# Kernel tuning notes

Hardware: AMD Instinct MI355X
Metric: run time of the kernel (lower is better)

## Reference

```python
import jax, jax.numpy as jnp
import numpy as np

COSIM_THRESHOLD = 0.5


def warp_affine_simple(src, theta, H, W):
    # src: [N, C, H, W], theta: [N, 2, 3]. Matches torch affine_grid+grid_sample
    # with align_corners=True and zero padding.
    ys = jnp.linspace(-1.0, 1.0, H)
    xs = jnp.linspace(-1.0, 1.0, W)
    gy, gx = jnp.meshgrid(ys, xs, indexing='ij')              # [H, W]
    base = jnp.stack([gx, gy, jnp.ones_like(gx)], axis=-1)    # [H, W, 3]
    coords = jnp.einsum('nij,hwj->nhwi', theta, base)         # [N, H, W, 2] (x, y)
    x = (coords[..., 0] + 1.0) * (W - 1) / 2.0
    y = (coords[..., 1] + 1.0) * (H - 1) / 2.0
    x0 = jnp.floor(x); y0 = jnp.floor(y)
    x1 = x0 + 1.0;     y1 = y0 + 1.0

    def corner(xi, yi):
        valid = ((xi >= 0) & (xi <= W - 1) & (yi >= 0) & (yi <= H - 1)).astype(src.dtype)
        xc = jnp.clip(xi, 0, W - 1).astype(jnp.int32)
        yc = jnp.clip(yi, 0, H - 1).astype(jnp.int32)
        vals = jax.vmap(lambda img, yy, xx: img[:, yy, xx])(src, yc, xc)  # [N, C, H, W]
        return vals * valid[:, None, :, :]

    wa = ((x1 - x) * (y1 - y))[:, None]
    wb = ((x - x0) * (y1 - y))[:, None]
    wc = ((x1 - x) * (y - y0))[:, None]
    wd = ((x - x0) * (y - y0))[:, None]
    return (corner(x0, y0) * wa + corner(x1, y0) * wb
            + corner(x0, y1) * wc + corner(x1, y1) * wd)


def setup_inputs() -> dict:
    key = jax.random.key(0)
    k1, k2, k3, k4 = jax.random.split(key, 4)
    B, N, nc, C, H, W = 4, 2, 256, 256, 96, 192
    feature = jax.random.normal(k1, (B * N, C, H, W), dtype=jnp.float32)
    codebook = jax.random.normal(k2, (nc, C), dtype=jnp.float32)
    codebook_pub = jax.random.normal(k3, (nc, C), dtype=jnp.float32)
    eye = jnp.broadcast_to(jnp.array([[1.0, 0.0, 0.0], [0.0, 1.0, 0.0]], jnp.float32),
                           (B, N, N, 2, 3))
    affine_matrix = eye + 0.05 * jax.random.normal(k4, (B, N, N, 2, 3), dtype=jnp.float32)
    record_len = jnp.full((B,), N, dtype=jnp.int32)
    return {'feature': feature, 'codebook': codebook, 'codebook_pub': codebook_pub,
            'affine_matrix': affine_matrix, 'record_len': record_len}


def reference(feature, codebook, codebook_pub, affine_matrix, record_len):
    # ---- sender: codebook dot-product weight projection + sigmoid ----
    # (local2unify / recombiner_send treated as identity: C == C_uni)
    b, C, H, W = feature.shape
    nc = codebook.shape[0]
    B = affine_matrix.shape[0]
    N = int(np.asarray(record_len)[0])  # uniform groups (static)

    dots = jnp.einsum('bchw,nc->bnhw', feature, codebook)           # [b, nc, H, W]
    norms = jnp.sum(codebook * codebook, axis=1)                    # [nc]
    weights = jax.nn.sigmoid(dots / norms[None, :, None, None])

    # ---- seletc_fill_weight: cosine-sim mask + affine-warp selective fill ----
    nl = codebook / jnp.linalg.norm(codebook, axis=1, keepdims=True)
    npub = codebook_pub / jnp.linalg.norm(codebook_pub, axis=1, keepdims=True)
    max_cosims = jnp.max(nl @ npub.T, axis=1)                       # [nc]
    masked = max_cosims <= COSIM_THRESHOLD                          # [nc]

    w = weights.reshape(B, N, nc, H, W)
    agent = jnp.arange(N)
    zero_cond = masked[None, None, :] & (agent[None, :, None] > 0)  # [1, N, nc]
    w = jnp.where(zero_cond[:, :, :, None, None], 0.0, w)

    # warp ego weights into each agent frame: t_matrix[:, i=0]
    theta = affine_matrix[:, :N, 0].reshape(B * N, 2, 3)
    ego = jnp.broadcast_to(w[:, :1], (B, N, nc, H, W)).reshape(B * N, nc, H, W)
    ego_w = warp_affine_simple(ego, theta, H, W).reshape(B, N, nc, H, W)

    w_sum = w.sum(axis=(-1, -2))                                    # [B, N, nc]
    fill = (w_sum == 0) & (agent[None, :, None] > 0)
    w = jnp.where(fill[:, :, :, None, None], ego_w, w)
    weights = w.reshape(b, nc, H, W)

    # ---- receiver: softmax over codes + einsum combine ----
    # (recombiner_receive / unify2local treated as identity)
    weights = jax.nn.softmax(weights, axis=1)
    out = jnp.einsum('bnhw,nc->bchw', weights, codebook)            # [b, C, H, W]
    return out
```

## Files before the change

### kernel.cpp

```cpp
#include <hip/hip_runtime.h>

#define HH 96
#define WW 192
#define PP (HH*WW)
#define CC 256
#define NCODE 256
#define NIMG 8
#define PT 64
#define PTILES (PP/PT)

typedef unsigned short u16;
typedef unsigned int u32;
using short8 = __attribute__((ext_vector_type(8))) short;
using f32x4  = __attribute__((ext_vector_type(4))) float;

__device__ inline u16 f2bf(float f) {
    union { float f; u32 u; } x; x.f = f;
    u32 r = x.u + 0x7fffu + ((x.u >> 16) & 1u);
    return (u16)(r >> 16);
}
__device__ inline float bf2f(u16 b) {
    union { u32 u; float f; } x; x.u = ((u32)b) << 16;
    return x.f;
}

__global__ __launch_bounds__(256) void k_prep(const float* __restrict__ cb,
                                              const float* __restrict__ cbp,
                                              float* __restrict__ invnorms,
                                              int*   __restrict__ masked,
                                              u16*   __restrict__ cbF,
                                              u16*   __restrict__ cbTF) {
    __shared__ float cbn[256];
    __shared__ float red[256];
    int n = blockIdx.x, t = threadIdx.x;
    float v = cb[n*256 + t];
    cbn[t] = v;
    red[t] = v * v;
    __syncthreads();
    for (int s = 128; s > 0; s >>= 1) { if (t < s) red[t] += red[t+s]; __syncthreads(); }
    float norm2 = red[0];
    if (t == 0) invnorms[n] = 1.0f / norm2;
    __syncthreads();

    {
        int ks = t >> 5, g = (t >> 3) & 3, j = t & 7;
        cbF[((size_t)(ks*16 + (n >> 4))*64 + g*16 + (n & 15))*8 + j] = f2bf(cbn[ks*32 + g*8 + j]);
    }
    {
        int ct = t >> 4, cl = t & 15;
        int ks = n >> 5, g = (n >> 3) & 3, j = n & 7;
        cbTF[((size_t)(ks*16 + ct)*64 + g*16 + cl)*8 + j] = f2bf(cbn[ct*16 + cl]);
    }
    float dot = 0.f, np2 = 0.f;
    const float4* pm4 = (const float4*)(cbp + (size_t)t*256);
    for (int c4 = 0; c4 < 64; ++c4) {
        float4 pv = pm4[c4];
        dot += cbn[c4*4+0]*pv.x + cbn[c4*4+1]*pv.y + cbn[c4*4+2]*pv.z + cbn[c4*4+3]*pv.w;
        np2 += pv.x*pv.x + pv.y*pv.y + pv.z*pv.z + pv.w*pv.w;
    }
    float cosv = dot * rsqrtf(norm2 * np2);
    __syncthreads();
    red[t] = cosv;
    __syncthreads();
    for (int s = 128; s > 0; s >>= 1) { if (t < s) red[t] = fmaxf(red[t], red[t+s]); __syncthreads(); }
    if (t == 0) masked[n] = (red[0] <= 0.5f) ? 1 : 0;
}

__global__ __launch_bounds__(256, 2) void k_gemm1f(const float* __restrict__ feat,
                                                   const u16* __restrict__ cbF,
                                                   const float* __restrict__ invnorms,
                                                   u16* __restrict__ w_all) {
    __shared__ alignas(16) u16 alds[32*64*8];
    int bid = blockIdx.x;
    int img = bid / PTILES, pt = bid % PTILES;
    int p0 = pt * PT;
    int t = threadIdx.x, wv = t >> 6, l = t & 63;
    int lr = l & 15, lg = l >> 4;

    short8 breg[32];
    #pragma unroll
    for (int nt = 0; nt < 4; ++nt)
        #pragma unroll
        for (int ks = 0; ks < 8; ++ks)
            breg[nt*8 + ks] = *(const short8*)(cbF + ((size_t)((ks*16 + wv*4 + nt)*64 + l))*8);

    float invn[4];
    #pragma unroll
    for (int nt = 0; nt < 4; ++nt) invn[nt] = invnorms[wv*64 + nt*16 + lr];

    int px = t & 63;
    int cgrp = t >> 6;
    const float* fb = feat + ((size_t)img*CC)*PP + p0 + px;
    int m_ = px >> 4;
    int lslot = px & 15;
    #pragma unroll
    for (int i = 0; i < 16; ++i) {
        int c0 = i*16 + cgrp*4;
        float f0 = fb[(size_t)(c0+0)*PP];
        float f1 = fb[(size_t)(c0+1)*PP];
        float f2 = fb[(size_t)(c0+2)*PP];
        float f3 = fb[(size_t)(c0+3)*PP];
        u32 lo = (u32)f2bf(f0) | ((u32)f2bf(f1) << 16);
        u32 hi = (u32)f2bf(f2) | ((u32)f2bf(f3) << 16);
        int ks = c0 >> 5;
        int lane = lslot + (((c0 >> 3) & 3) << 4);
        u32* dst = (u32*)((char*)alds + ((size_t)((m_*8 + ks)*64 + lane))*16 + (c0 & 7)*2);
        dst[0] = lo; dst[1] = hi;
    }
    __syncthreads();

    #pragma unroll
    for (int m = 0; m < 4; ++m) {
        f32x4 acc[4];
        #pragma unroll
        for (int nt = 0; nt < 4; ++nt) acc[nt] = (f32x4){0.f,0.f,0.f,0.f};
        #pragma unroll
        for (int ks = 0; ks < 8; ++ks) {
            short8 a = *(const short8*)(alds + ((size_t)((m*8 + ks)*64 + l))*8);
            #pragma unroll
            for (int nt = 0; nt < 4; ++nt)
                acc[nt] = __builtin_amdgcn_mfma_f32_16x16x32_bf16(a, breg[nt*8 + ks], acc[nt], 0, 0, 0);
        }
        #pragma unroll
        for (int nt = 0; nt < 4; ++nt) {
            #pragma unroll
            for (int r = 0; r < 4; ++r) {
                int p = p0 + m*16 + lg*4 + r;
                int n = wv*64 + nt*16 + lr;
                float x = acc[nt][r] * invn[nt];
                float w = 1.f / (1.f + __expf(-x));
                w_all[((size_t)img*PP + p)*256 + n] = f2bf(w);
            }
        }
    }
}

__global__ __launch_bounds__(256, 2) void k_out(const u16* __restrict__ w_all,
                                                const u16* __restrict__ cbTF,
                                                const int* __restrict__ masked,
                                                const float* __restrict__ am,
                                                float* __restrict__ out) {
    __shared__ alignas(16) u16 smx[32*64*8];
    int bid = blockIdx.x;
    int img = bid / PTILES, pt = bid % PTILES;
    int p0 = pt * PT;
    int t = threadIdx.x;

    {
        int pl = t >> 2, q = t & 3;
        int p = p0 + pl;
        float vals[64];
        const u16* own = w_all + ((size_t)img*PP + p)*256 + q*64;
        #pragma unroll
        for (int i = 0; i < 8; ++i) {
            short8 v = *(const short8*)(own + i*8);
            #pragma unroll
            for (int j = 0; j < 8; ++j) vals[i*8 + j] = bf2f((u16)v[j]);
        }
        if (img & 1) {
            int hh = p / WW, ww = p % WW;
            const float* th = am + (size_t)img*12;
            float gx = ww * (2.f/(WW-1)) - 1.f;
            float gy = hh * (2.f/(HH-1)) - 1.f;
            float xr = th[0]*gx + th[1]*gy + th[2];
            float yr = th[3]*gx + th[4]*gy + th[5];
            float x = (xr + 1.f) * ((WW-1)*0.5f);
            float y = (yr + 1.f) * ((HH-1)*0.5f);
            float x0f = floorf(x), y0f = floorf(y);
            float dx = x - x0f, dy = y - y0f;
            int x0 = (int)x0f, y0 = (int)y0f;
            float wc4[4] = {(1.f-dx)*(1.f-dy), dx*(1.f-dy), (1.f-dx)*dy, dx*dy};
            int xs_[4] = {x0, x0+1, x0, x0+1};
            int ys_[4] = {y0, y0, y0+1, y0+1};
            const u16* w0 = w_all + ((size_t)(img-1)*PP)*256;
            const u16* cptr[4];
            #pragma unroll
            for (int k = 0; k < 4; ++k) {
                bool ok = (xs_[k] >= 0) & (xs_[k] < WW) & (ys_[k] >= 0) & (ys_[k] < HH);
                cptr[k] = ok ? (w0 + ((size_t)(ys_[k]*WW + xs_[k]))*256 + q*64) : nullptr;
            }
            #pragma unroll
            for (int ch = 0; ch < 4; ++ch) {
                float wch[16];
                #pragma unroll
                for (int i = 0; i < 16; ++i) wch[i] = 0.f;
                #pragma unroll
                for (int k = 0; k < 4; ++k) {
                    if (cptr[k]) {
                        const u16* cp = cptr[k] + ch*16;
                        short8 a = *(const short8*)(cp);
                        short8 b = *(const short8*)(cp + 8);
                        float wk = wc4[k];
                        #pragma unroll
                        for (int j = 0; j < 8; ++j) { wch[j] += wk*bf2f((u16)a[j]); wch[8+j] += wk*bf2f((u16)b[j]); }
                    }
                }
                #pragma unroll
                for (int i = 0; i < 16; ++i)
                    if (masked[q*64 + ch*16 + i]) vals[ch*16 + i] = wch[i];
            }
        }
        float m = vals[0];
        #pragma unroll
        for (int i = 1; i < 64; ++i) m = fmaxf(m, vals[i]);
        m = fmaxf(m, __shfl_xor(m, 1));
        m = fmaxf(m, __shfl_xor(m, 2));
        float s = 0.f;
        #pragma unroll
        for (int i = 0; i < 64; ++i) { vals[i] = __expf(vals[i] - m); s += vals[i]; }
        s += __shfl_xor(s, 1);
        s += __shfl_xor(s, 2);
        float inv = 1.f / s;
        int p4 = pl >> 4;
        #pragma unroll
        for (int i = 0; i < 32; ++i) {
            int n = q*64 + i*2;
            int ks = n >> 5;
            int lane = (pl & 15) + (((n >> 3) & 3) << 4);
            u32 v = (u32)f2bf(vals[i*2] * inv) | ((u32)f2bf(vals[i*2+1] * inv) << 16);
            *(u32*)((char*)smx + ((size_t)((ks*4 + p4)*64 + lane))*16 + (n & 7)*2) = v;
        }
    }

    int wv = t >> 6, l = t & 63;
    int lr = l & 15, lg = l >> 4;
    short8 areg[32];
    #pragma unroll
    for (int ct = 0; ct < 4; ++ct)
        #pragma unroll
        for (int ks = 0; ks < 8; ++ks)
            areg[ct*8 + ks] = *(const short8*)(cbTF + ((size_t)((ks*16 + wv*4 + ct)*64 + l))*8);
    __syncthreads();

    f32x4 acc[4][4];
    #pragma unroll
    for (int i = 0; i < 4; ++i)
        #pragma unroll
        for (int j = 0; j < 4; ++j) acc[i][j] = (f32x4){0.f,0.f,0.f,0.f};

    #pragma unroll
    for (int ks = 0; ks < 8; ++ks) {
        short8 b[4];
        #pragma unroll
        for (int p4 = 0; p4 < 4; ++p4)
            b[p4] = *(const short8*)(smx + ((size_t)((ks*4 + p4)*64 + l))*8);
        #pragma unroll
        for (int ct = 0; ct < 4; ++ct)
            #pragma unroll
            for (int p4 = 0; p4 < 4; ++p4)
                acc[ct][p4] = __builtin_amdgcn_mfma_f32_16x16x32_bf16(areg[ct*8 + ks], b[p4], acc[ct][p4], 0, 0, 0);
    }
    #pragma unroll
    for (int ct = 0; ct < 4; ++ct)
        #pragma unroll
        for (int p4 = 0; p4 < 4; ++p4)
            #pragma unroll
            for (int r = 0; r < 4; ++r) {
                int c = wv*64 + ct*16 + lg*4 + r;
                int p = p0 + p4*16 + lr;
                out[((size_t)img*CC + c)*PP + p] = acc[ct][p4][r];
            }
}

extern "C" void kernel_launch(void* const* d_in, const int* in_sizes, int n_in,
                              void* d_out, int out_size, void* d_ws, size_t ws_size,
                              hipStream_t stream) {
    const float* feature = (const float*)d_in[0];
    const float* cb      = (const float*)d_in[1];
    const float* cbp     = (const float*)d_in[2];
    const float* am      = (const float*)d_in[3];
    float* out = (float*)d_out;

    char* ws = (char*)d_ws;
    size_t o = 0;
    u16* w_all = (u16*)(ws + o); o += (size_t)NIMG*PP*NCODE*2;
    u16* cbF   = (u16*)(ws + o); o += 256*256*2;
    u16* cbTF  = (u16*)(ws + o); o += 256*256*2;
    float* invnorms = (float*)(ws + o); o += 256*4;
    int* masked     = (int*)(ws + o);   o += 256*4;

    hipLaunchKernelGGL(k_prep, dim3(256), dim3(256), 0, stream, cb, cbp, invnorms, masked, cbF, cbTF);
    hipLaunchKernelGGL(k_gemm1f, dim3(NIMG*PTILES), dim3(256), 0, stream, feature, cbF, invnorms, w_all);
    hipLaunchKernelGGL(k_out, dim3(NIMG*PTILES), dim3(256), 0, stream, w_all, cbTF, masked, am, out);
}
```

Measured before the change: 351.5 us.

## Skip agent GEMM when all codes masked, pack mask bits, raise occupancy

k_prep now writes a count of unmasked codes plus a 256-bit mask bitset. When every code is masked, k_gemm1f skips the non-ego images and k_out zero-fills their own weights instead of loading them. Register use is cut by splitting B/A fragments into two halves so launch bounds can go to 3 blocks per CU. The softmax tile in LDS now uses a row-major layout with XOR swizzling and 16-byte stores. The skip depends on the data: with random codebooks the max cosine is likely below 0.5 for all codes, so the skip path probably runs on the test inputs. The semantics stay correct in either case.

```diff
diff --git a/kernel.cpp b/kernel.cpp
--- a/kernel.cpp
+++ b/kernel.cpp
@@ -27,7 +27,7 @@
 __global__ __launch_bounds__(256) void k_prep(const float* __restrict__ cb,
                                               const float* __restrict__ cbp,
                                               float* __restrict__ invnorms,
-                                              int*   __restrict__ masked,
+                                              int*   __restrict__ meta,
                                               u16*   __restrict__ cbF,
                                               u16*   __restrict__ cbTF) {
     __shared__ float cbn[256];
@@ -63,30 +63,32 @@
     red[t] = cosv;
     __syncthreads();
     for (int s = 128; s > 0; s >>= 1) { if (t < s) red[t] = fmaxf(red[t], red[t+s]); __syncthreads(); }
-    if (t == 0) masked[n] = (red[0] <= 0.5f) ? 1 : 0;
-}
-
-__global__ __launch_bounds__(256, 2) void k_gemm1f(const float* __restrict__ feat,
+    if (t == 0) {
+        int maskedv = (red[0] <= 0.5f) ? 1 : 0;
+        if (maskedv) atomicOr((u32*)&meta[1 + (n >> 5)], 1u << (n & 31));
+        else         atomicAdd(&meta[0], 1);
+    }
+}
+
+__global__ __launch_bounds__(256, 3) void k_gemm1f(const float* __restrict__ feat,
                                                    const u16* __restrict__ cbF,
                                                    const float* __restrict__ invnorms,
-                                                   u16* __restrict__ w_all) {
+                                                   u16* __restrict__ w_all,
+                                                   const int* __restrict__ meta) {
     __shared__ alignas(16) u16 alds[32*64*8];
     int bid = blockIdx.x;
     int img = bid / PTILES, pt = bid % PTILES;
+    if ((img & 1) && (meta[0] == 0)) return;
     int p0 = pt * PT;
     int t = threadIdx.x, wv = t >> 6, l = t & 63;
     int lr = l & 15, lg = l >> 4;
 
-    short8 breg[32];
+    short8 breg[16];
     #pragma unroll
-    for (int nt = 0; nt < 4; ++nt)
+    for (int nt2 = 0; nt2 < 2; ++nt2)
         #pragma unroll
         for (int ks = 0; ks < 8; ++ks)
-            breg[nt*8 + ks] = *(const short8*)(cbF + ((size_t)((ks*16 + wv*4 + nt)*64 + l))*8);
-
-    float invn[4];
-    #pragma unroll
-    for (int nt = 0; nt < 4; ++nt) invn[nt] = invnorms[wv*64 + nt*16 + lr];
+            breg[nt2*8 + ks] = *(const short8*)(cbF + ((size_t)((ks*16 + wv*4 + nt2)*64 + l))*8);
 
     int px = t & 63;
     int cgrp = t >> 6;
@@ -110,52 +112,76 @@
     __syncthreads();
 
     #pragma unroll
-    for (int m = 0; m < 4; ++m) {
-        f32x4 acc[4];
-        #pragma unroll
-        for (int nt = 0; nt < 4; ++nt) acc[nt] = (f32x4){0.f,0.f,0.f,0.f};
-        #pragma unroll
-        for (int ks = 0; ks < 8; ++ks) {
-            short8 a = *(const short8*)(alds + ((size_t)((m*8 + ks)*64 + l))*8);
-            #pragma unroll
-            for (int nt = 0; nt < 4; ++nt)
-                acc[nt] = __builtin_amdgcn_mfma_f32_16x16x32_bf16(a, breg[nt*8 + ks], acc[nt], 0, 0, 0);
-        }
-        #pragma unroll
-        for (int nt = 0; nt < 4; ++nt) {
-            #pragma unroll
-            for (int r = 0; r < 4; ++r) {
-                int p = p0 + m*16 + lg*4 + r;
-                int n = wv*64 + nt*16 + lr;
-                float x = acc[nt][r] * invn[nt];
-                float w = 1.f / (1.f + __expf(-x));
-                w_all[((size_t)img*PP + p)*256 + n] = f2bf(w);
-            }
-        }
-    }
-}
-
-__global__ __launch_bounds__(256, 2) void k_out(const u16* __restrict__ w_all,
+    for (int nh = 0; nh < 2; ++nh) {
+        if (nh) {
+            #pragma unroll
+            for (int nt2 = 0; nt2 < 2; ++nt2)
+                #pragma unroll
+                for (int ks = 0; ks < 8; ++ks)
+                    breg[nt2*8 + ks] = *(const short8*)(cbF + ((size_t)((ks*16 + wv*4 + 2 + nt2)*64 + l))*8);
+        }
+        float invn[2];
+        #pragma unroll
+        for (int nt2 = 0; nt2 < 2; ++nt2) invn[nt2] = invnorms[wv*64 + (nh*2 + nt2)*16 + lr];
+        #pragma unroll
+        for (int m = 0; m < 4; ++m) {
+            f32x4 acc[2];
+            acc[0] = (f32x4){0.f,0.f,0.f,0.f};
+            acc[1] = (f32x4){0.f,0.f,0.f,0.f};
+            #pragma unroll
+            for (int ks = 0; ks < 8; ++ks) {
+                short8 a = *(const short8*)(alds + ((size_t)((m*8 + ks)*64 + l))*8);
+                acc[0] = __builtin_amdgcn_mfma_f32_16x16x32_bf16(a, breg[ks],     acc[0], 0, 0, 0);
+                acc[1] = __builtin_amdgcn_mfma_f32_16x16x32_bf16(a, breg[8 + ks], acc[1], 0, 0, 0);
+            }
+            #pragma unroll
+            for (int nt2 = 0; nt2 < 2; ++nt2) {
+                #pragma unroll
+                for (int r = 0; r < 4; ++r) {
+                    int p = p0 + m*16 + lg*4 + r;
+                    int n = wv*64 + (nh*2 + nt2)*16 + lr;
+                    float x = acc[nt2][r] * invn[nt2];
+                    float w = 1.f / (1.f + __expf(-x));
+                    w_all[((size_t)img*PP + p)*256 + n] = f2bf(w);
+                }
+            }
+        }
+    }
+}
+
+__device__ inline u32 smx_off(int p, int n) {
+    return (u32)(((p*256 + n)*2) ^ ((p & 7) << 4));
+}
+
+__global__ __launch_bounds__(256, 3) void k_out(const u16* __restrict__ w_all,
                                                 const u16* __restrict__ cbTF,
-                                                const int* __restrict__ masked,
+                                                const int* __restrict__ meta,
                                                 const float* __restrict__ am,
                                                 float* __restrict__ out) {
-    __shared__ alignas(16) u16 smx[32*64*8];
+    __shared__ alignas(16) u16 smx[64*256];
     int bid = blockIdx.x;
     int img = bid / PTILES, pt = bid % PTILES;
     int p0 = pt * PT;
     int t = threadIdx.x;
+    bool allm = (meta[0] == 0);
 
     {
         int pl = t >> 2, q = t & 3;
         int p = p0 + pl;
+        u32 mb0 = (u32)meta[1 + q*2], mb1 = (u32)meta[2 + q*2];
+        bool ego_only = (img & 1) && allm;
         float vals[64];
-        const u16* own = w_all + ((size_t)img*PP + p)*256 + q*64;
-        #pragma unroll
-        for (int i = 0; i < 8; ++i) {
-            short8 v = *(const short8*)(own + i*8);
-            #pragma unroll
-            for (int j = 0; j < 8; ++j) vals[i*8 + j] = bf2f((u16)v[j]);
+        if (!ego_only) {
+            const u16* own = w_all + ((size_t)img*PP + p)*256 + q*64;
+            #pragma unroll
+            for (int i = 0; i < 8; ++i) {
+                short8 v = *(const short8*)(own + i*8);
+                #pragma unroll
+                for (int j = 0; j < 8; ++j) vals[i*8 + j] = bf2f((u16)v[j]);
+            }
+        } else {
+            #pragma unroll
+            for (int i = 0; i < 64; ++i) vals[i] = 0.f;
         }
         if (img & 1) {
             int hh = p / WW, ww = p % WW;
@@ -195,9 +221,12 @@
                         for (int j = 0; j < 8; ++j) { wch[j] += wk*bf2f((u16)a[j]); wch[8+j] += wk*bf2f((u16)b[j]); }
                     }
                 }
-                #pragma unroll
-                for (int i = 0; i < 16; ++i)
-                    if (masked[q*64 + ch*16 + i]) vals[ch*16 + i] = wch[i];
+                u32 mb = (ch < 2) ? mb0 : mb1;
+                #pragma unroll
+                for (int i = 0; i < 16; ++i) {
+                    int bit = (ch & 1)*16 + i;
+                    if ((mb >> bit) & 1) vals[ch*16 + i] = wch[i];
+                }
             }
         }
         float m = vals[0];
@@ -211,55 +240,54 @@
         s += __shfl_xor(s, 1);
         s += __shfl_xor(s, 2);
         float inv = 1.f / s;
-        int p4 = pl >> 4;
-        #pragma unroll
-        for (int i = 0; i < 32; ++i) {
-            int n = q*64 + i*2;
-            int ks = n >> 5;
-            int lane = (pl & 15) + (((n >> 3) & 3) << 4);
-            u32 v = (u32)f2bf(vals[i*2] * inv) | ((u32)f2bf(vals[i*2+1] * inv) << 16);
-            *(u32*)((char*)smx + ((size_t)((ks*4 + p4)*64 + lane))*16 + (n & 7)*2) = v;
-        }
-    }
+        #pragma unroll
+        for (int i = 0; i < 8; ++i) {
+            short8 v;
+            #pragma unroll
+            for (int j = 0; j < 8; ++j) v[j] = (short)f2bf(vals[i*8 + j] * inv);
+            *(short8*)((char*)smx + smx_off(pl, q*64 + i*8)) = v;
+        }
+    }
+    __syncthreads();
 
     int wv = t >> 6, l = t & 63;
     int lr = l & 15, lg = l >> 4;
-    short8 areg[32];
     #pragma unroll
-    for (int ct = 0; ct < 4; ++ct)
-        #pragma unroll
-        for (int ks = 0; ks < 8; ++ks)
-            areg[ct*8 + ks] = *(const short8*)(cbTF + ((size_t)((ks*16 + wv*4 + ct)*64 + l))*8);
-    __syncthreads();
-
-    f32x4 acc[4][4];
-    #pragma unroll
-    for (int i = 0; i < 4; ++i)
-        #pragma unroll
-        for (int j = 0; j < 4; ++j) acc[i][j] = (f32x4){0.f,0.f,0.f,0.f};
-
-    #pragma unroll
-    for (int ks = 0; ks < 8; ++ks) {
-        short8 b[4];
-        #pragma unroll
-        for (int p4 = 0; p4 < 4; ++p4)
-            b[p4] = *(const short8*)(smx + ((size_t)((ks*4 + p4)*64 + l))*8);
-        #pragma unroll
-        for (int ct = 0; ct < 4; ++ct)
+    for (int ch = 0; ch < 2; ++ch) {
+        short8 areg[16];
+        #pragma unroll
+        for (int ct2 = 0; ct2 < 2; ++ct2)
+            #pragma unroll
+            for (int ks = 0; ks < 8; ++ks)
+                areg[ct2*8 + ks] = *(const short8*)(cbTF + ((size_t)((ks*16 + wv*4 + ch*2 + ct2)*64 + l))*8);
+        f32x4 acc[2][4];
+        #pragma unroll
+        for (int i = 0; i < 2; ++i)
+            #pragma unroll
+            for (int j = 0; j < 4; ++j) acc[i][j] = (f32x4){0.f,0.f,0.f,0.f};
+        #pragma unroll
+        for (int ks = 0; ks < 8; ++ks) {
+            short8 b[4];
             #pragma unroll
             for (int p4 = 0; p4 < 4; ++p4)
-                acc[ct][p4] = __builtin_amdgcn_mfma_f32_16x16x32_bf16(areg[ct*8 + ks], b[p4], acc[ct][p4], 0, 0, 0);
-    }
-    #pragma unroll
-    for (int ct = 0; ct < 4; ++ct)
-        #pragma unroll
-        for (int p4 = 0; p4 < 4; ++p4)
-            #pragma unroll
-            for (int r = 0; r < 4; ++r) {
-                int c = wv*64 + ct*16 + lg*4 + r;
-                int p = p0 + p4*16 + lr;
-                out[((size_t)img*CC + c)*PP + p] = acc[ct][p4][r];
-            }
+                b[p4] = *(const short8*)((char*)smx + smx_off(p4*16 + lr, ks*32 + lg*8));
+            #pragma unroll
+            for (int ct2 = 0; ct2 < 2; ++ct2)
+                #pragma unroll
+                for (int p4 = 0; p4 < 4; ++p4)
+                    acc[ct2][p4] = __builtin_amdgcn_mfma_f32_16x16x32_bf16(areg[ct2*8 + ks], b[p4], acc[ct2][p4], 0, 0, 0);
+        }
+        #pragma unroll
+        for (int ct2 = 0; ct2 < 2; ++ct2)
+            #pragma unroll
+            for (int p4 = 0; p4 < 4; ++p4)
+                #pragma unroll
+                for (int r = 0; r < 4; ++r) {
+                    int c = wv*64 + (ch*2 + ct2)*16 + lg*4 + r;
+                    int p = p0 + p4*16 + lr;
+                    out[((size_t)img*CC + c)*PP + p] = acc[ct2][p4][r];
+                }
+    }
 }
 
 extern "C" void kernel_launch(void* const* d_in, const int* in_sizes, int n_in,
@@ -277,9 +305,10 @@
     u16* cbF   = (u16*)(ws + o); o += 256*256*2;
     u16* cbTF  = (u16*)(ws + o); o += 256*256*2;
     float* invnorms = (float*)(ws + o); o += 256*4;
-    int* masked     = (int*)(ws + o);   o += 256*4;
-
-    hipLaunchKernelGGL(k_prep, dim3(256), dim3(256), 0, stream, cb, cbp, invnorms, masked, cbF, cbTF);
-    hipLaunchKernelGGL(k_gemm1f, dim3(NIMG*PTILES), dim3(256), 0, stream, feature, cbF, invnorms, w_all);
-    hipLaunchKernelGGL(k_out, dim3(NIMG*PTILES), dim3(256), 0, stream, w_all, cbTF, masked, am, out);
-}
+    int* meta       = (int*)(ws + o);   o += 9*4;
+
+    hipMemsetAsync(meta, 0, 9*4, stream);
+    hipLaunchKernelGGL(k_prep, dim3(256), dim3(256), 0, stream, cb, cbp, invnorms, meta, cbF, cbTF);
+    hipLaunchKernelGGL(k_gemm1f, dim3(NIMG*PTILES), dim3(256), 0, stream, feature, cbF, invnorms, w_all, meta);
+    hipLaunchKernelGGL(k_out, dim3(NIMG*PTILES), dim3(256), 0, stream, w_all, cbTF, meta, am, out);
+}
```

New measurement: 332.6 us. -5.4%, faster.
